# Kernel optimization log

Hardware: AMD Instinct MI355X
Metric: run time of the kernel (lower is better)

Reference implementation:

```python
import jax, jax.numpy as jnp
import numpy as np

N_NODES = 100000
IN_FEAT, HID, OUT_FEAT, GRID = 128, 64, 40, 8
N_EDGES = 1600000


def spmm(row, col, w, x):
    # out[i] = sum_{e: row[e]==i} w[e] * x[col[e]]
    return jax.ops.segment_sum(w[:, None] * x[col], row, num_segments=N_NODES)


def kan_layer(x, coeff):
    # coeff: [2, out, in, grid]; Fourier KAN: y[b,j] = sum_{i,k} cos(k x_bi) C0[j,i,k] + sin(k x_bi) C1[j,i,k]
    grid = coeff.shape[-1]
    k = jnp.arange(1, grid + 1, dtype=x.dtype)  # [G]
    ang = x[:, :, None] * k  # [N, in, G]
    y = jnp.einsum('bik,jik->bj', jnp.cos(ang), coeff[0])
    y = y + jnp.einsum('bik,jik->bj', jnp.sin(ang), coeff[1])
    return y


def setup_inputs() -> dict:
    key = jax.random.key(0)
    ks = jax.random.split(key, 8)
    scale = 1.0 / (np.sqrt(HID) * np.sqrt(GRID))
    return {
        'x': jax.random.normal(ks[0], (N_NODES, IN_FEAT), dtype=jnp.float32),
        'edge_row': jax.random.randint(ks[1], (N_EDGES,), 0, N_NODES),
        'edge_col': jax.random.randint(ks[2], (N_EDGES,), 0, N_NODES),
        'edge_weight': jax.random.uniform(ks[3], (N_EDGES,), dtype=jnp.float32),
        'W_in': jax.random.normal(ks[4], (IN_FEAT, HID), dtype=jnp.float32) / np.sqrt(IN_FEAT),
        'b_in': jnp.zeros((HID,), dtype=jnp.float32),
        'coeffs1': jax.random.normal(ks[5], (2, HID, HID, GRID), dtype=jnp.float32) * scale,
        'coeffs2': jax.random.normal(ks[6], (2, HID, HID, GRID), dtype=jnp.float32) * scale,
        'W_out': jax.random.normal(ks[7], (HID, OUT_FEAT), dtype=jnp.float32) / np.sqrt(HID),
    }


def reference(x, edge_row, edge_col, edge_weight, W_in, b_in, coeffs1, coeffs2, W_out):
    h = x @ W_in + b_in                                  # lin_in
    h = kan_layer(spmm(edge_row, edge_col, edge_weight, h), coeffs1)
    h = kan_layer(spmm(edge_row, edge_col, edge_weight, h), coeffs2)
    out = h @ W_out                                      # final bias-free linear
    return jax.nn.log_softmax(out, axis=-1)
```

## Files before the change

kernel.cpp:

```cpp
#include <hip/hip_runtime.h>
#include <hip/hip_bf16.h>
#include <string.h>


#define N_NODES 100000
#define IN_FEAT 128
#define HID 64
#define OUT_FEAT 40
#define NGRID 8
#define N_EDGES 1600000
#define NELEM (N_NODES * HID)

#define NB 98
#define CAP 18432
#define BCHUNK 4096
#define BIN_BLOCKS ((N_EDGES + BCHUNK - 1) / BCHUNK)

using short8 = __attribute__((ext_vector_type(8))) short;
using floatx4 = __attribute__((ext_vector_type(4))) float;
using uintx4 = __attribute__((ext_vector_type(4))) unsigned;

#define GLOAD_LDS16(gp, lp)                                                   \
  __builtin_amdgcn_global_load_lds(                                           \
      (const __attribute__((address_space(1))) unsigned*)(gp),                \
      (__attribute__((address_space(3))) unsigned*)(lp), 16, 0, 0)

__device__ __forceinline__ unsigned pack_bf16x2(float c, float s) {
  unsigned uc = __float_as_uint(c);
  unsigned us = __float_as_uint(s);
  uc += 0x7fffu + ((uc >> 16) & 1u);
  us += 0x7fffu + ((us >> 16) & 1u);
  return (uc >> 16) | (us & 0xffff0000u);
}

__device__ __forceinline__ unsigned cvtpk_bf16x2(float c, float s) {
  __hip_bfloat162 p = __float22bfloat162_rn(make_float2(c, s));
  unsigned r;
  memcpy(&r, &p, 4);
  return r;
}

__global__ __launch_bounds__(256) void lin_in_kernel(
    const float* __restrict__ x, const float* __restrict__ W,
    const float* __restrict__ b, float* __restrict__ h) {
  __shared__ __align__(16) float xs[16 * IN_FEAT];
  int t = threadIdx.x;
  int nb = blockIdx.x;
  const float4* xsrc = (const float4*)(x + (size_t)nb * 16 * IN_FEAT);
  float4* xd = (float4*)xs;
  xd[t] = xsrc[t];
  xd[t + 256] = xsrc[t + 256];
  __syncthreads();
  int lane = t & 63, wv = t >> 6;
  float bj = b[lane];
  float a0 = bj, a1 = bj, a2 = bj, a3 = bj;
  const float* xr = xs + wv * 4 * IN_FEAT;
  const float* Wj = W + lane;
#pragma unroll 4
  for (int i4 = 0; i4 < 32; i4++) {
    float4 x0 = *(const float4*)(xr + 0 * IN_FEAT + i4 * 4);
    float4 x1 = *(const float4*)(xr + 1 * IN_FEAT + i4 * 4);
    float4 x2 = *(const float4*)(xr + 2 * IN_FEAT + i4 * 4);
    float4 x3 = *(const float4*)(xr + 3 * IN_FEAT + i4 * 4);
    float w0 = Wj[(i4 * 4 + 0) * HID];
    float w1 = Wj[(i4 * 4 + 1) * HID];
    float w2 = Wj[(i4 * 4 + 2) * HID];
    float w3 = Wj[(i4 * 4 + 3) * HID];
    a0 = fmaf(x0.x, w0, a0); a0 = fmaf(x0.y, w1, a0); a0 = fmaf(x0.z, w2, a0); a0 = fmaf(x0.w, w3, a0);
    a1 = fmaf(x1.x, w0, a1); a1 = fmaf(x1.y, w1, a1); a1 = fmaf(x1.z, w2, a1); a1 = fmaf(x1.w, w3, a1);
    a2 = fmaf(x2.x, w0, a2); a2 = fmaf(x2.y, w1, a2); a2 = fmaf(x2.z, w2, a2); a2 = fmaf(x2.w, w3, a2);
    a3 = fmaf(x3.x, w0, a3); a3 = fmaf(x3.y, w1, a3); a3 = fmaf(x3.z, w2, a3); a3 = fmaf(x3.w, w3, a3);
  }
  size_t nbase = (size_t)nb * 16 + wv * 4;
  h[(nbase + 0) * HID + lane] = a0;
  h[(nbase + 1) * HID + lane] = a1;
  h[(nbase + 2) * HID + lane] = a2;
  h[(nbase + 3) * HID + lane] = a3;
}

__global__ __launch_bounds__(128) void binit_kernel(int* __restrict__ btail) {
  int t = threadIdx.x;
  if (t < NB) btail[t] = t * CAP;
}

__global__ __launch_bounds__(256) void bin_kernel(
    const int* __restrict__ row, const int* __restrict__ col,
    const float* __restrict__ w, int* __restrict__ btail,
    uint2* __restrict__ pack1) {
  __shared__ __align__(16) uint2 stage[BCHUNK];
  __shared__ int bcnt[NB];
  __shared__ int lbase[NB];
  __shared__ int gbase[NB];
  __shared__ int lcur[NB];
  __shared__ int sc[128];
  int t = threadIdx.x;
  int e0 = blockIdx.x * BCHUNK;
  if (t < NB) bcnt[t] = 0;
  __syncthreads();
  int rloc[16];
#pragma unroll
  for (int q = 0; q < 16; q++) {
    int e = e0 + q * 256 + t;
    int r = (e < N_EDGES) ? row[e] : -1;
    rloc[q] = r;
    if (r >= 0) atomicAdd(&bcnt[r >> 10], 1);
  }
  __syncthreads();
  int c = (t < NB) ? bcnt[t] : 0;
  if (t < 128) sc[t] = c;
  __syncthreads();
  int v = c;
#pragma unroll
  for (int off = 1; off < 128; off <<= 1) {
    int add = (t >= off && t < 128) ? sc[t - off] : 0;
    __syncthreads();
    if (t < 128) sc[t] = v = v + add;
    __syncthreads();
  }
  if (t < NB) {
    lbase[t] = v - c;
    lcur[t] = v - c;
    gbase[t] = atomicAdd(&btail[t], c);
  }
  __syncthreads();
#pragma unroll
  for (int q = 0; q < 16; q++) {
    int e = e0 + q * 256 + t;
    int r = rloc[q];
    if (r >= 0) {
      int p = atomicAdd(&lcur[r >> 10], 1);
      unsigned key = ((unsigned)(r & 1023) << 17) | (unsigned)col[e];
      stage[p] = make_uint2(key, __float_as_uint(w[e]));
    }
  }
  __syncthreads();
  int wv = t >> 6, lane = t & 63;
  for (int b = wv; b < NB; b += 4) {
    int len = bcnt[b], src = lbase[b];
    uint2* dst = pack1 + (size_t)gbase[b];
    for (int i = lane; i < len; i += 64)
      dst[i] = stage[src + i];
  }
}

__global__ __launch_bounds__(256) void bucket_finalize_kernel(
    const int* __restrict__ btail, const uint2* __restrict__ pack1,
    int* __restrict__ rowptr, uint2* __restrict__ pack2) {
  __shared__ int rcnt[1024];
  __shared__ int sc[256];
  __shared__ int binfo[2];
  int b = blockIdx.x, t = threadIdx.x;
  if (t < NB) sc[t] = btail[t] - t * CAP;
  rcnt[t] = 0; rcnt[t + 256] = 0; rcnt[t + 512] = 0; rcnt[t + 768] = 0;
  __syncthreads();
  if (t == 0) {
    int base = 0;
    for (int i = 0; i < b; i++) base += sc[i];
    binfo[0] = base;
    binfo[1] = sc[b];
  }
  __syncthreads();
  int base = binfo[0], len = binfo[1];
  const uint2* rec = pack1 + (size_t)b * CAP;
  for (int i = t; i < len; i += 256)
    atomicAdd(&rcnt[rec[i].x >> 17], 1);
  __syncthreads();
  int c0 = rcnt[4 * t], c1 = rcnt[4 * t + 1], c2 = rcnt[4 * t + 2], c3 = rcnt[4 * t + 3];
  int s4 = c0 + c1 + c2 + c3;
  sc[t] = s4;
  __syncthreads();
  int v = s4;
#pragma unroll
  for (int off = 1; off < 256; off <<= 1) {
    int add = (t >= off) ? sc[t - off] : 0;
    __syncthreads();
    sc[t] = v = v + add;
    __syncthreads();
  }
  int excl = v - s4;
  int p0 = base + excl;
  int p1 = p0 + c0, p2 = p1 + c1, p3 = p2 + c2;
  int r0 = (b << 10) + 4 * t;
  if (r0 + 0 < N_NODES) rowptr[r0 + 0] = p0;
  if (r0 + 1 < N_NODES) rowptr[r0 + 1] = p1;
  if (r0 + 2 < N_NODES) rowptr[r0 + 2] = p2;
  if (r0 + 3 < N_NODES) rowptr[r0 + 3] = p3;
  rcnt[4 * t] = p0; rcnt[4 * t + 1] = p1; rcnt[4 * t + 2] = p2; rcnt[4 * t + 3] = p3;
  __syncthreads();
  for (int i = t; i < len; i += 256) {
    uint2 p = rec[i];
    int pos = atomicAdd(&rcnt[p.x >> 17], 1);
    pack2[pos] = make_uint2(p.x & 0x1FFFFu, p.y);
  }
  if (b == NB - 1 && t == 0) rowptr[N_NODES] = N_EDGES;
}

__global__ __launch_bounds__(256) void spmm_csr_kernel(
    const int* __restrict__ rowptr, const uint2* __restrict__ pack,
    const float* __restrict__ h, float* __restrict__ acc) {
  int wv = threadIdx.x >> 6, lane = threadIdx.x & 63;
  int n = blockIdx.x * 4 + wv;
  int beg = rowptr[n], end = rowptr[n + 1];
  int slot = lane >> 4, f4 = lane & 15;
  const float4* h4 = (const float4*)h;
  const unsigned long long* packq = (const unsigned long long*)pack;
  float4 v = make_float4(0.f, 0.f, 0.f, 0.f);
  for (int e = beg; e < end; e += 16) {
    int i0 = e + slot, i1 = i0 + 4, i2 = i0 + 8, i3 = i0 + 12;
    int c0 = i0 < end ? i0 : end - 1;
    int c1 = i1 < end ? i1 : end - 1;
    int c2 = i2 < end ? i2 : end - 1;
    int c3 = i3 < end ? i3 : end - 1;
    unsigned long long p0 = __builtin_nontemporal_load(packq + c0);
    unsigned long long p1 = __builtin_nontemporal_load(packq + c1);
    unsigned long long p2 = __builtin_nontemporal_load(packq + c2);
    unsigned long long p3 = __builtin_nontemporal_load(packq + c3);
    float4 h0 = h4[(size_t)(unsigned)p0 * 16 + f4];
    float4 h1 = h4[(size_t)(unsigned)p1 * 16 + f4];
    float4 h2 = h4[(size_t)(unsigned)p2 * 16 + f4];
    float4 h3 = h4[(size_t)(unsigned)p3 * 16 + f4];
    float w0 = (i0 < end) ? __uint_as_float((unsigned)(p0 >> 32)) : 0.f;
    float w1 = (i1 < end) ? __uint_as_float((unsigned)(p1 >> 32)) : 0.f;
    float w2 = (i2 < end) ? __uint_as_float((unsigned)(p2 >> 32)) : 0.f;
    float w3 = (i3 < end) ? __uint_as_float((unsigned)(p3 >> 32)) : 0.f;
    v.x = fmaf(w0, h0.x, v.x); v.y = fmaf(w0, h0.y, v.y);
    v.z = fmaf(w0, h0.z, v.z); v.w = fmaf(w0, h0.w, v.w);
    v.x = fmaf(w1, h1.x, v.x); v.y = fmaf(w1, h1.y, v.y);
    v.z = fmaf(w1, h1.z, v.z); v.w = fmaf(w1, h1.w, v.w);
    v.x = fmaf(w2, h2.x, v.x); v.y = fmaf(w2, h2.y, v.y);
    v.z = fmaf(w2, h2.z, v.z); v.w = fmaf(w2, h2.w, v.w);
    v.x = fmaf(w3, h3.x, v.x); v.y = fmaf(w3, h3.y, v.y);
    v.z = fmaf(w3, h3.z, v.z); v.w = fmaf(w3, h3.w, v.w);
  }
#pragma unroll
  for (int off = 16; off < 64; off <<= 1) {
    v.x += __shfl_xor(v.x, off);
    v.y += __shfl_xor(v.y, off);
    v.z += __shfl_xor(v.z, off);
    v.w += __shfl_xor(v.w, off);
  }
  if (slot == 0) {
    floatx4 vv = {v.x, v.y, v.z, v.w};
    __builtin_nontemporal_store(vv, (floatx4*)acc + (size_t)n * 16 + f4);
  }
}

__global__ __launch_bounds__(256) void repack_kernel(
    const float* __restrict__ coeffs, unsigned* __restrict__ Brep) {
  int idx = blockIdx.x * 256 + threadIdx.x;
  int ch = idx >> 13;
  int rem = idx & 8191;
  int blk = rem >> 8;
  int jt = blk >> 3, ks = blk & 7;
  int rem2 = rem & 255;
  int ls = rem2 >> 2;
  int quad = ls >> 4, m_n = ls & 15;
  int jj = rem2 & 3;
  int j = jt * 16 + m_n;
  int r = ks >> 1, km1 = ((ks & 1) << 2) | jj;
  int i = ch * 16 + quad * 4 + r;
  int ws = i * 8 + km1;
  float c0 = coeffs[(size_t)j * 512 + ws];
  float c1 = coeffs[32768 + (size_t)j * 512 + ws];
  Brep[idx] = pack_bf16x2(c0, c1);
}

__global__ __launch_bounds__(256, 4) void kan_mfma_kernel(
    const float* __restrict__ s, const unsigned* __restrict__ Brep,
    float* __restrict__ out) {
  __shared__ __align__(16) unsigned Bs[2][4096];
  int t = threadIdx.x;
  int lane = t & 63;
  int wv = t >> 6;
  int nb = blockIdx.x;

  int m_n = lane & 15;
  int quad = lane >> 4;
  int node_sub = wv * 16 + m_n;
  int n_row = nb * 64 + node_sub;
  bool rvalid = (n_row < N_NODES);

  const char* Gb = (const char*)Brep;

#pragma unroll
  for (int i = 0; i < 4; i++) {
    int c = i * 4 + wv;
    GLOAD_LDS16(Gb + c * 1024 + lane * 16, (char*)&Bs[0][0] + c * 1024);
  }

  float4 sv[4];
#pragma unroll
  for (int ch = 0; ch < 4; ch++) {
    sv[ch] = rvalid
      ? *reinterpret_cast<const float4*>(s + (size_t)n_row * HID + ch * 16 + quad * 4)
      : make_float4(0.f, 0.f, 0.f, 0.f);
  }

  floatx4 acc[4];
#pragma unroll
  for (int jt = 0; jt < 4; jt++) acc[jt] = (floatx4){0.f, 0.f, 0.f, 0.f};

  short8 afr[8];

#pragma unroll
  for (int h = 0; h < 8; h++) {
    asm volatile("s_waitcnt vmcnt(0)" ::: "memory");
    __syncthreads();

    if (h < 7) {
      const char* gsrc = Gb + (h + 1) * 16384;
      char* ldst = (char*)&Bs[(h + 1) & 1][0];
#pragma unroll
      for (int i = 0; i < 4; i++) {
        int c = i * 4 + wv;
        GLOAD_LDS16(gsrc + c * 1024 + lane * 16, ldst + c * 1024);
      }
    }

    if ((h & 1) == 0) {
      int ch = h >> 1;
      float ss[4] = {sv[ch].x, sv[ch].y, sv[ch].z, sv[ch].w};
#pragma unroll
      for (int r = 0; r < 4; r++) {
        float s1, c1;
        __sincosf(ss[r], &s1, &c1);
        float ck = c1, sk = s1;
        unsigned wbuf[8];
#pragma unroll
        for (int km1 = 0; km1 < 8; km1++) {
          wbuf[km1] = cvtpk_bf16x2(ck, sk);
          float cn = fmaf(ck, c1, -sk * s1);
          float sn = fmaf(sk, c1, ck * s1);
          ck = cn; sk = sn;
        }
        uintx4 lo = (uintx4){wbuf[0], wbuf[1], wbuf[2], wbuf[3]};
        uintx4 hi = (uintx4){wbuf[4], wbuf[5], wbuf[6], wbuf[7]};
        memcpy(&afr[2 * r], &lo, 16);
        memcpy(&afr[2 * r + 1], &hi, 16);
      }
    }

    const char* Bb = (const char*)&Bs[h & 1][0];
    int jtp = (h & 1) * 2;
#pragma unroll
    for (int ks = 0; ks < 8; ks++) {
      short8 af = afr[ks];
#pragma unroll
      for (int j2 = 0; j2 < 2; j2++) {
        short8 bf = *reinterpret_cast<const short8*>(Bb + (j2 * 8 + ks) * 1024 + lane * 16);
        acc[jtp + j2] = __builtin_amdgcn_mfma_f32_16x16x32_bf16(af, bf, acc[jtp + j2], 0, 0, 0);
      }
    }
  }

#pragma unroll
  for (int jt = 0; jt < 4; jt++) {
#pragma unroll
    for (int reg = 0; reg < 4; reg++) {
      int node = nb * 64 + wv * 16 + quad * 4 + reg;
      if (node < N_NODES)
        out[(size_t)node * HID + jt * 16 + m_n] = acc[jt][reg];
    }
  }
}

__global__ __launch_bounds__(256, 2) void final_kernel(
    const float* __restrict__ h, const float* __restrict__ Wout,
    float* __restrict__ out) {
  __shared__ __align__(16) float hs[64 * HID];
  int t = threadIdx.x;
  int lane = t & 63, wv = t >> 6;
  int nb = blockIdx.x;
  bool jvalid = lane < OUT_FEAT;
  int jc = jvalid ? lane : 0;

  float wl[HID];
#pragma unroll
  for (int i = 0; i < HID; i++)
    wl[i] = Wout[i * OUT_FEAT + jc];

  const float4* hsrc = (const float4*)(h + (size_t)nb * 64 * HID);
  float4* hd = (float4*)hs;
#pragma unroll
  for (int q = 0; q < 4; q++)
    hd[q * 256 + t] = hsrc[q * 256 + t];
  __syncthreads();

  int nwbase = nb * 64 + wv * 16;
  for (int ns = 0; ns < 16; ns += 2) {
    const float* h0 = hs + (wv * 16 + ns) * HID;
    const float* h1 = h0 + HID;
    float d0 = 0.f, d1 = 0.f;
#pragma unroll
    for (int i4 = 0; i4 < 16; i4++) {
      float4 a = *(const float4*)(h0 + i4 * 4);
      float4 b = *(const float4*)(h1 + i4 * 4);
      d0 = fmaf(a.x, wl[i4 * 4 + 0], d0);  d1 = fmaf(b.x, wl[i4 * 4 + 0], d1);
      d0 = fmaf(a.y, wl[i4 * 4 + 1], d0);  d1 = fmaf(b.y, wl[i4 * 4 + 1], d1);
      d0 = fmaf(a.z, wl[i4 * 4 + 2], d0);  d1 = fmaf(b.z, wl[i4 * 4 + 2], d1);
      d0 = fmaf(a.w, wl[i4 * 4 + 3], d0);  d1 = fmaf(b.w, wl[i4 * 4 + 3], d1);
    }
    float m0 = jvalid ? d0 : -1e30f;
    float m1 = jvalid ? d1 : -1e30f;
#pragma unroll
    for (int off = 32; off; off >>= 1) {
      m0 = fmaxf(m0, __shfl_xor(m0, off));
      m1 = fmaxf(m1, __shfl_xor(m1, off));
    }
    float e0 = jvalid ? expf(d0 - m0) : 0.f;
    float e1 = jvalid ? expf(d1 - m1) : 0.f;
    float s0 = e0, s1 = e1;
#pragma unroll
    for (int off = 32; off; off >>= 1) {
      s0 += __shfl_xor(s0, off);
      s1 += __shfl_xor(s1, off);
    }
    float l0 = m0 + logf(s0);
    float l1 = m1 + logf(s1);
    int n0 = nwbase + ns, n1 = n0 + 1;
    if (jvalid) {
      if (n0 < N_NODES) out[(size_t)n0 * OUT_FEAT + lane] = d0 - l0;
      if (n1 < N_NODES) out[(size_t)n1 * OUT_FEAT + lane] = d1 - l1;
    }
  }
}

extern "C" void kernel_launch(void* const* d_in, const int* in_sizes, int n_in,
                              void* d_out, int out_size, void* d_ws, size_t ws_size,
                              hipStream_t stream) {
  (void)in_sizes; (void)n_in; (void)out_size; (void)ws_size;
  const float* x    = (const float*)d_in[0];
  const int*   erow = (const int*)d_in[1];
  const int*   ecol = (const int*)d_in[2];
  const float* ew   = (const float*)d_in[3];
  const float* W_in = (const float*)d_in[4];
  const float* b_in = (const float*)d_in[5];
  const float* c1   = (const float*)d_in[6];
  const float* c2   = (const float*)d_in[7];
  const float* Wout = (const float*)d_in[8];
  float* out = (float*)d_out;

  float* h   = (float*)d_ws;
  float* acc = h + NELEM;

  unsigned* xw     = (unsigned*)(void*)x;
  unsigned* Brep1  = xw;
  unsigned* Brep2  = xw + 32768;
  int*      btail  = (int*)(xw + 65536);
  int*      rowptr = (int*)(xw + 66048);
  uint2*    pack1  = (uint2*)(xw + 262144);
  uint2*    pack2  = (uint2*)(xw + 3932160);

  lin_in_kernel<<<N_NODES / 16, 256, 0, stream>>>(x, W_in, b_in, h);

  repack_kernel<<<128, 256, 0, stream>>>(c1, Brep1);
  repack_kernel<<<128, 256, 0, stream>>>(c2, Brep2);

  binit_kernel<<<1, 128, 0, stream>>>(btail);
  bin_kernel<<<BIN_BLOCKS, 256, 0, stream>>>(erow, ecol, ew, btail, pack1);
  bucket_finalize_kernel<<<NB, 256, 0, stream>>>(btail, pack1, rowptr, pack2);

  spmm_csr_kernel<<<N_NODES / 4, 256, 0, stream>>>(rowptr, pack2, h, acc);
  kan_mfma_kernel<<<(N_NODES + 63) / 64, 256, 0, stream>>>(acc, Brep1, h);

  spmm_csr_kernel<<<N_NODES / 4, 256, 0, stream>>>(rowptr, pack2, h, acc);
  kan_mfma_kernel<<<(N_NODES + 63) / 64, 256, 0, stream>>>(acc, Brep2, h);

  final_kernel<<<(N_NODES + 63) / 64, 256, 0, stream>>>(h, Wout, out);
}
```

Baseline: 435.1 us.

## Fuse SpMM gather with KAN MFMA layer and final linear/log-softmax

Merges each SpMM pass with its following KAN MFMA layer into one kernel. The aggregated features for a 64-node tile stay in LDS, so the intermediate acc buffer is never written to or read back from global memory. The second fused instance also does the final linear and log-softmax, which removes the separate final kernel and its read of h. To save LDS, B-coefficient staging is split into smaller 8KB double-buffered chunks over 16 steps. The cost is that the gather now runs in blocks limited by the MFMA kernel's occupancy, and each wave handles 16 rows in sequence, which may hide less latency than the old one-row-per-wave SpMM grid.

New measurement: 425.4 us. -2.2%, faster.

```diff
diff --git a/kernel.cpp b/kernel.cpp
--- a/kernel.cpp
+++ b/kernel.cpp
@@ -195,56 +195,6 @@
   if (b == NB - 1 && t == 0) rowptr[N_NODES] = N_EDGES;
 }
 
-__global__ __launch_bounds__(256) void spmm_csr_kernel(
-    const int* __restrict__ rowptr, const uint2* __restrict__ pack,
-    const float* __restrict__ h, float* __restrict__ acc) {
-  int wv = threadIdx.x >> 6, lane = threadIdx.x & 63;
-  int n = blockIdx.x * 4 + wv;
-  int beg = rowptr[n], end = rowptr[n + 1];
-  int slot = lane >> 4, f4 = lane & 15;
-  const float4* h4 = (const float4*)h;
-  const unsigned long long* packq = (const unsigned long long*)pack;
-  float4 v = make_float4(0.f, 0.f, 0.f, 0.f);
-  for (int e = beg; e < end; e += 16) {
-    int i0 = e + slot, i1 = i0 + 4, i2 = i0 + 8, i3 = i0 + 12;
-    int c0 = i0 < end ? i0 : end - 1;
-    int c1 = i1 < end ? i1 : end - 1;
-    int c2 = i2 < end ? i2 : end - 1;
-    int c3 = i3 < end ? i3 : end - 1;
-    unsigned long long p0 = __builtin_nontemporal_load(packq + c0);
-    unsigned long long p1 = __builtin_nontemporal_load(packq + c1);
-    unsigned long long p2 = __builtin_nontemporal_load(packq + c2);
-    unsigned long long p3 = __builtin_nontemporal_load(packq + c3);
-    float4 h0 = h4[(size_t)(unsigned)p0 * 16 + f4];
-    float4 h1 = h4[(size_t)(unsigned)p1 * 16 + f4];
-    float4 h2 = h4[(size_t)(unsigned)p2 * 16 + f4];
-    float4 h3 = h4[(size_t)(unsigned)p3 * 16 + f4];
-    float w0 = (i0 < end) ? __uint_as_float((unsigned)(p0 >> 32)) : 0.f;
-    float w1 = (i1 < end) ? __uint_as_float((unsigned)(p1 >> 32)) : 0.f;
-    float w2 = (i2 < end) ? __uint_as_float((unsigned)(p2 >> 32)) : 0.f;
-    float w3 = (i3 < end) ? __uint_as_float((unsigned)(p3 >> 32)) : 0.f;
-    v.x = fmaf(w0, h0.x, v.x); v.y = fmaf(w0, h0.y, v.y);
-    v.z = fmaf(w0, h0.z, v.z); v.w = fmaf(w0, h0.w, v.w);
-    v.x = fmaf(w1, h1.x, v.x); v.y = fmaf(w1, h1.y, v.y);
-    v.z = fmaf(w1, h1.z, v.z); v.w = fmaf(w1, h1.w, v.w);
-    v.x = fmaf(w2, h2.x, v.x); v.y = fmaf(w2, h2.y, v.y);
-    v.z = fmaf(w2, h2.z, v.z); v.w = fmaf(w2, h2.w, v.w);
-    v.x = fmaf(w3, h3.x, v.x); v.y = fmaf(w3, h3.y, v.y);
-    v.z = fmaf(w3, h3.z, v.z); v.w = fmaf(w3, h3.w, v.w);
-  }
-#pragma unroll
-  for (int off = 16; off < 64; off <<= 1) {
-    v.x += __shfl_xor(v.x, off);
-    v.y += __shfl_xor(v.y, off);
-    v.z += __shfl_xor(v.z, off);
-    v.w += __shfl_xor(v.w, off);
-  }
-  if (slot == 0) {
-    floatx4 vv = {v.x, v.y, v.z, v.w};
-    __builtin_nontemporal_store(vv, (floatx4*)acc + (size_t)n * 16 + f4);
-  }
-}
-
 __global__ __launch_bounds__(256) void repack_kernel(
     const float* __restrict__ coeffs, unsigned* __restrict__ Brep) {
   int idx = blockIdx.x * 256 + threadIdx.x;
@@ -265,60 +215,102 @@
   Brep[idx] = pack_bf16x2(c0, c1);
 }
 
-__global__ __launch_bounds__(256, 4) void kan_mfma_kernel(
-    const float* __restrict__ s, const unsigned* __restrict__ Brep,
-    float* __restrict__ out) {
-  __shared__ __align__(16) unsigned Bs[2][4096];
+template <int DO_FINAL>
+__global__ __launch_bounds__(256, 4) void fused_spmm_kan_kernel(
+    const int* __restrict__ rowptr, const uint2* __restrict__ pack,
+    const float* __restrict__ hin, const unsigned* __restrict__ Brep,
+    float* __restrict__ outp, const float* __restrict__ Wout) {
+  __shared__ __align__(16) unsigned Bs[2][2048];
+  __shared__ __align__(16) float s_tile[64 * 64];
   int t = threadIdx.x;
-  int lane = t & 63;
-  int wv = t >> 6;
+  int lane = t & 63, wv = t >> 6;
   int nb = blockIdx.x;
-
-  int m_n = lane & 15;
-  int quad = lane >> 4;
+  const char* Gb = (const char*)Brep;
+
+#pragma unroll
+  for (int i = 0; i < 2; i++) {
+    int c = wv + 4 * i;
+    GLOAD_LDS16(Gb + c * 1024 + lane * 16, (char*)&Bs[0][0] + c * 1024);
+  }
+
+  {
+    int rpi = nb * 64 + wv * 16 + lane;
+    int rp = 0;
+    if (lane < 17) rp = rowptr[rpi < N_NODES ? rpi : N_NODES];
+    int slot = lane >> 4, f4 = lane & 15;
+    const float4* h4 = (const float4*)hin;
+    const unsigned long long* packq = (const unsigned long long*)pack;
+    for (int i = 0; i < 16; i++) {
+      int beg = __shfl(rp, i), end = __shfl(rp, i + 1);
+      float4 v = make_float4(0.f, 0.f, 0.f, 0.f);
+      for (int e = beg; e < end; e += 16) {
+        int i0 = e + slot, i1 = i0 + 4, i2 = i0 + 8, i3 = i0 + 12;
+        int c0 = i0 < end ? i0 : end - 1;
+        int c1 = i1 < end ? i1 : end - 1;
+        int c2 = i2 < end ? i2 : end - 1;
+        int c3 = i3 < end ? i3 : end - 1;
+        unsigned long long p0 = __builtin_nontemporal_load(packq + c0);
+        unsigned long long p1 = __builtin_nontemporal_load(packq + c1);
+        unsigned long long p2 = __builtin_nontemporal_load(packq + c2);
+        unsigned long long p3 = __builtin_nontemporal_load(packq + c3);
+        float4 h0 = h4[(size_t)(unsigned)p0 * 16 + f4];
+        float4 h1 = h4[(size_t)(unsigned)p1 * 16 + f4];
+        float4 h2 = h4[(size_t)(unsigned)p2 * 16 + f4];
+        float4 h3 = h4[(size_t)(unsigned)p3 * 16 + f4];
+        float w0 = (i0 < end) ? __uint_as_float((unsigned)(p0 >> 32)) : 0.f;
+        float w1 = (i1 < end) ? __uint_as_float((unsigned)(p1 >> 32)) : 0.f;
+        float w2 = (i2 < end) ? __uint_as_float((unsigned)(p2 >> 32)) : 0.f;
+        float w3 = (i3 < end) ? __uint_as_float((unsigned)(p3 >> 32)) : 0.f;
+        v.x = fmaf(w0, h0.x, v.x); v.y = fmaf(w0, h0.y, v.y);
+        v.z = fmaf(w0, h0.z, v.z); v.w = fmaf(w0, h0.w, v.w);
+        v.x = fmaf(w1, h1.x, v.x); v.y = fmaf(w1, h1.y, v.y);
+        v.z = fmaf(w1, h1.z, v.z); v.w = fmaf(w1, h1.w, v.w);
+        v.x = fmaf(w2, h2.x, v.x); v.y = fmaf(w2, h2.y, v.y);
+        v.z = fmaf(w2, h2.z, v.z); v.w = fmaf(w2, h2.w, v.w);
+        v.x = fmaf(w3, h3.x, v.x); v.y = fmaf(w3, h3.y, v.y);
+        v.z = fmaf(w3, h3.z, v.z); v.w = fmaf(w3, h3.w, v.w);
+      }
+#pragma unroll
+      for (int off = 16; off < 64; off <<= 1) {
+        v.x += __shfl_xor(v.x, off);
+        v.y += __shfl_xor(v.y, off);
+        v.z += __shfl_xor(v.z, off);
+        v.w += __shfl_xor(v.w, off);
+      }
+      if (slot == 0)
+        *(float4*)&s_tile[(wv * 16 + i) * 64 + f4 * 4] = v;
+    }
+  }
+  __syncthreads();
+
+  int m_n = lane & 15, quad = lane >> 4;
   int node_sub = wv * 16 + m_n;
-  int n_row = nb * 64 + node_sub;
-  bool rvalid = (n_row < N_NODES);
-
-  const char* Gb = (const char*)Brep;
-
-#pragma unroll
-  for (int i = 0; i < 4; i++) {
-    int c = i * 4 + wv;
-    GLOAD_LDS16(Gb + c * 1024 + lane * 16, (char*)&Bs[0][0] + c * 1024);
-  }
-
   float4 sv[4];
 #pragma unroll
-  for (int ch = 0; ch < 4; ch++) {
-    sv[ch] = rvalid
-      ? *reinterpret_cast<const float4*>(s + (size_t)n_row * HID + ch * 16 + quad * 4)
-      : make_float4(0.f, 0.f, 0.f, 0.f);
-  }
+  for (int ch = 0; ch < 4; ch++)
+    sv[ch] = *(const float4*)&s_tile[node_sub * 64 + ch * 16 + quad * 4];
 
   floatx4 acc[4];
 #pragma unroll
   for (int jt = 0; jt < 4; jt++) acc[jt] = (floatx4){0.f, 0.f, 0.f, 0.f};
-
   short8 afr[8];
 
 #pragma unroll
-  for (int h = 0; h < 8; h++) {
+  for (int q = 0; q < 16; q++) {
     asm volatile("s_waitcnt vmcnt(0)" ::: "memory");
     __syncthreads();
-
-    if (h < 7) {
-      const char* gsrc = Gb + (h + 1) * 16384;
-      char* ldst = (char*)&Bs[(h + 1) & 1][0];
-#pragma unroll
-      for (int i = 0; i < 4; i++) {
-        int c = i * 4 + wv;
+    if (q < 15) {
+      int qq = q + 1;
+      const char* gsrc = Gb + (qq >> 2) * 32768 + (qq & 3) * 8192;
+      char* ldst = (char*)&Bs[qq & 1][0];
+#pragma unroll
+      for (int i = 0; i < 2; i++) {
+        int c = wv + 4 * i;
         GLOAD_LDS16(gsrc + c * 1024 + lane * 16, ldst + c * 1024);
       }
     }
-
-    if ((h & 1) == 0) {
-      int ch = h >> 1;
+    if ((q & 3) == 0) {
+      int ch = q >> 2;
       float ss[4] = {sv[ch].x, sv[ch].y, sv[ch].z, sv[ch].w};
 #pragma unroll
       for (int r = 0; r < 4; r++) {
@@ -339,88 +331,75 @@
         memcpy(&afr[2 * r + 1], &hi, 16);
       }
     }
-
-    const char* Bb = (const char*)&Bs[h & 1][0];
-    int jtp = (h & 1) * 2;
+    const char* Bb = (const char*)&Bs[q & 1][0];
+    int jt = q & 3;
 #pragma unroll
     for (int ks = 0; ks < 8; ks++) {
-      short8 af = afr[ks];
-#pragma unroll
-      for (int j2 = 0; j2 < 2; j2++) {
-        short8 bf = *reinterpret_cast<const short8*>(Bb + (j2 * 8 + ks) * 1024 + lane * 16);
-        acc[jtp + j2] = __builtin_amdgcn_mfma_f32_16x16x32_bf16(af, bf, acc[jtp + j2], 0, 0, 0);
-      }
-    }
-  }
-
-#pragma unroll
-  for (int jt = 0; jt < 4; jt++) {
-#pragma unroll
-    for (int reg = 0; reg < 4; reg++) {
-      int node = nb * 64 + wv * 16 + quad * 4 + reg;
-      if (node < N_NODES)
-        out[(size_t)node * HID + jt * 16 + m_n] = acc[jt][reg];
-    }
-  }
-}
-
-__global__ __launch_bounds__(256, 2) void final_kernel(
-    const float* __restrict__ h, const float* __restrict__ Wout,
-    float* __restrict__ out) {
-  __shared__ __align__(16) float hs[64 * HID];
-  int t = threadIdx.x;
-  int lane = t & 63, wv = t >> 6;
-  int nb = blockIdx.x;
-  bool jvalid = lane < OUT_FEAT;
-  int jc = jvalid ? lane : 0;
-
-  float wl[HID];
-#pragma unroll
-  for (int i = 0; i < HID; i++)
-    wl[i] = Wout[i * OUT_FEAT + jc];
-
-  const float4* hsrc = (const float4*)(h + (size_t)nb * 64 * HID);
-  float4* hd = (float4*)hs;
-#pragma unroll
-  for (int q = 0; q < 4; q++)
-    hd[q * 256 + t] = hsrc[q * 256 + t];
-  __syncthreads();
-
-  int nwbase = nb * 64 + wv * 16;
-  for (int ns = 0; ns < 16; ns += 2) {
-    const float* h0 = hs + (wv * 16 + ns) * HID;
-    const float* h1 = h0 + HID;
-    float d0 = 0.f, d1 = 0.f;
-#pragma unroll
-    for (int i4 = 0; i4 < 16; i4++) {
-      float4 a = *(const float4*)(h0 + i4 * 4);
-      float4 b = *(const float4*)(h1 + i4 * 4);
-      d0 = fmaf(a.x, wl[i4 * 4 + 0], d0);  d1 = fmaf(b.x, wl[i4 * 4 + 0], d1);
-      d0 = fmaf(a.y, wl[i4 * 4 + 1], d0);  d1 = fmaf(b.y, wl[i4 * 4 + 1], d1);
-      d0 = fmaf(a.z, wl[i4 * 4 + 2], d0);  d1 = fmaf(b.z, wl[i4 * 4 + 2], d1);
-      d0 = fmaf(a.w, wl[i4 * 4 + 3], d0);  d1 = fmaf(b.w, wl[i4 * 4 + 3], d1);
-    }
-    float m0 = jvalid ? d0 : -1e30f;
-    float m1 = jvalid ? d1 : -1e30f;
-#pragma unroll
-    for (int off = 32; off; off >>= 1) {
-      m0 = fmaxf(m0, __shfl_xor(m0, off));
-      m1 = fmaxf(m1, __shfl_xor(m1, off));
-    }
-    float e0 = jvalid ? expf(d0 - m0) : 0.f;
-    float e1 = jvalid ? expf(d1 - m1) : 0.f;
-    float s0 = e0, s1 = e1;
-#pragma unroll
-    for (int off = 32; off; off >>= 1) {
-      s0 += __shfl_xor(s0, off);
-      s1 += __shfl_xor(s1, off);
-    }
-    float l0 = m0 + logf(s0);
-    float l1 = m1 + logf(s1);
-    int n0 = nwbase + ns, n1 = n0 + 1;
-    if (jvalid) {
-      if (n0 < N_NODES) out[(size_t)n0 * OUT_FEAT + lane] = d0 - l0;
-      if (n1 < N_NODES) out[(size_t)n1 * OUT_FEAT + lane] = d1 - l1;
+      short8 bf = *reinterpret_cast<const short8*>(Bb + ks * 1024 + lane * 16);
+      acc[jt] = __builtin_amdgcn_mfma_f32_16x16x32_bf16(afr[ks], bf, acc[jt], 0, 0, 0);
+    }
+  }
+
+  if (DO_FINAL == 0) {
+#pragma unroll
+    for (int jt = 0; jt < 4; jt++) {
+#pragma unroll
+      for (int reg = 0; reg < 4; reg++) {
+        int node = nb * 64 + wv * 16 + quad * 4 + reg;
+        if (node < N_NODES)
+          outp[(size_t)node * HID + jt * 16 + m_n] = acc[jt][reg];
+      }
+    }
+  } else {
+#pragma unroll
+    for (int jt = 0; jt < 4; jt++) {
+#pragma unroll
+      for (int reg = 0; reg < 4; reg++)
+        s_tile[(wv * 16 + quad * 4 + reg) * 64 + jt * 16 + m_n] = acc[jt][reg];
+    }
+    __syncthreads();
+    bool jvalid = lane < OUT_FEAT;
+    int jc = jvalid ? lane : 0;
+    float wl[HID];
+#pragma unroll
+    for (int i2 = 0; i2 < HID; i2++)
+      wl[i2] = Wout[i2 * OUT_FEAT + jc];
+    int nwbase = nb * 64 + wv * 16;
+    for (int ns = 0; ns < 16; ns += 2) {
+      const float* h0p = &s_tile[(wv * 16 + ns) * 64];
+      const float* h1p = h0p + 64;
+      float d0 = 0.f, d1 = 0.f;
+#pragma unroll
+      for (int i4 = 0; i4 < 16; i4++) {
+        float4 a = *(const float4*)(h0p + i4 * 4);
+        float4 b = *(const float4*)(h1p + i4 * 4);
+        d0 = fmaf(a.x, wl[i4 * 4 + 0], d0);  d1 = fmaf(b.x, wl[i4 * 4 + 0], d1);
+        d0 = fmaf(a.y, wl[i4 * 4 + 1], d0);  d1 = fmaf(b.y, wl[i4 * 4 + 1], d1);
+        d0 = fmaf(a.z, wl[i4 * 4 + 2], d0);  d1 = fmaf(b.z, wl[i4 * 4 + 2], d1);
+        d0 = fmaf(a.w, wl[i4 * 4 + 3], d0);  d1 = fmaf(b.w, wl[i4 * 4 + 3], d1);
+      }
+      float m0 = jvalid ? d0 : -1e30f;
+      float m1 = jvalid ? d1 : -1e30f;
+#pragma unroll
+      for (int off = 32; off; off >>= 1) {
+        m0 = fmaxf(m0, __shfl_xor(m0, off));
+        m1 = fmaxf(m1, __shfl_xor(m1, off));
+      }
+      float e0 = jvalid ? expf(d0 - m0) : 0.f;
+      float e1 = jvalid ? expf(d1 - m1) : 0.f;
+      float s0 = e0, s1 = e1;
+#pragma unroll
+      for (int off = 32; off; off >>= 1) {
+        s0 += __shfl_xor(s0, off);
+        s1 += __shfl_xor(s1, off);
+      }
+      float l0 = m0 + logf(s0);
+      float l1 = m1 + logf(s1);
+      int n0 = nwbase + ns, n1 = n0 + 1;
+      if (jvalid) {
+        if (n0 < N_NODES) outp[(size_t)n0 * OUT_FEAT + lane] = d0 - l0;
+        if (n1 < N_NODES) outp[(size_t)n1 * OUT_FEAT + lane] = d1 - l1;
+      }
     }
   }
 }
@@ -440,8 +419,8 @@
   const float* Wout = (const float*)d_in[8];
   float* out = (float*)d_out;
 
-  float* h   = (float*)d_ws;
-  float* acc = h + NELEM;
+  float* h0 = (float*)d_ws;
+  float* h1 = h0 + NELEM;
 
   unsigned* xw     = (unsigned*)(void*)x;
   unsigned* Brep1  = xw;
@@ -451,7 +430,9 @@
   uint2*    pack1  = (uint2*)(xw + 262144);
   uint2*    pack2  = (uint2*)(xw + 3932160);
 
-  lin_in_kernel<<<N_NODES / 16, 256, 0, stream>>>(x, W_in, b_in, h);
+  const int fgrid = (N_NODES + 63) / 64;
+
+  lin_in_kernel<<<N_NODES / 16, 256, 0, stream>>>(x, W_in, b_in, h0);
 
   repack_kernel<<<128, 256, 0, stream>>>(c1, Brep1);
   repack_kernel<<<128, 256, 0, stream>>>(c2, Brep2);
@@ -460,11 +441,8 @@
   bin_kernel<<<BIN_BLOCKS, 256, 0, stream>>>(erow, ecol, ew, btail, pack1);
   bucket_finalize_kernel<<<NB, 256, 0, stream>>>(btail, pack1, rowptr, pack2);
 
-  spmm_csr_kernel<<<N_NODES / 4, 256, 0, stream>>>(rowptr, pack2, h, acc);
-  kan_mfma_kernel<<<(N_NODES + 63) / 64, 256, 0, stream>>>(acc, Brep1, h);
-
-  spmm_csr_kernel<<<N_NODES / 4, 256, 0, stream>>>(rowptr, pack2, h, acc);
-  kan_mfma_kernel<<<(N_NODES + 63) / 64, 256, 0, stream>>>(acc, Brep2, h);
-
-  final_kernel<<<(N_NODES + 63) / 64, 256, 0, stream>>>(h, Wout, out);
-}
+  fused_spmm_kan_kernel<0><<<fgrid, 256, 0, stream>>>(
+      rowptr, pack2, h0, Brep1, h1, nullptr);
+  fused_spmm_kan_kernel<1><<<fgrid, 256, 0, stream>>>(
+      rowptr, pack2, h1, Brep2, out, Wout);
+}
```
